# Performance work log

Hardware: AMD Instinct MI355X
Metric: run time of the kernel (lower is better)

The kernel has to match this reference:

```python
import jax, jax.numpy as jnp
import numpy as np

D = 1024          # input_dim
H = 16            # num_heads
S = 2             # scalar
MAX_LEN = 2048
HEAD_DIM = D // H // S      # 32
DV = D // H                 # 64, value head dim
SCALING = (D // H) ** -0.5


def setup_inputs() -> dict:
    key = jax.random.key(0)
    k1, k2, k3, k4, k5, k6 = jax.random.split(key, 6)
    L, B = 2046, 4
    input_tensor = jax.random.normal(k1, (L, B, D), dtype=jnp.float32)
    # k_v_proj: Linear(MAX_LEN, MAX_LEN // S); bias exists but is unused in forward
    w_kv = jax.random.normal(k2, (MAX_LEN // S, MAX_LEN), dtype=jnp.float32) / np.sqrt(MAX_LEN)
    # q_proj: Linear(D, D // S)
    w_q = jax.random.normal(k3, (D // S, D), dtype=jnp.float32) / np.sqrt(D)
    b_q = jax.random.normal(k4, (D // S,), dtype=jnp.float32) * 0.01
    # out_proj: Linear(D, D)
    w_out = jax.random.normal(k5, (D, D), dtype=jnp.float32) / np.sqrt(D)
    b_out = jax.random.normal(k6, (D,), dtype=jnp.float32) * 0.01
    return {"input_tensor": input_tensor, "w_kv": w_kv, "w_q": w_q,
            "b_q": b_q, "w_out": w_out, "b_out": b_out}


def reference(input_tensor, w_kv, w_q, b_q, w_out, b_out):
    L, B, _ = input_tensor.shape
    P = L // S + 1                       # projected (low-rank) sequence length
    X = jnp.transpose(input_tensor, (1, 0, 2))        # [B, L, D]
    q = X @ w_q.T + b_q                                # [B, L, D/S]
    Wp = w_kv.T[:L, :P]                                # [L, P] sequence projection
    v = jnp.einsum('bld,lp->bdp', X, Wp)               # [B, D, P]
    k = jnp.einsum('blc,lp->bcp', q, Wp)               # [B, D/S, P]
    q = q * SCALING
    # q: b l (h d) -> b h l d
    qh = q.reshape(B, L, H, HEAD_DIM).transpose(0, 2, 1, 3)
    # k: b (d h) p -> b h d p   (d outer, h inner in the channel split)
    kh = k.reshape(B, HEAD_DIM, H, P).transpose(0, 2, 1, 3)
    # v: b (d h) p -> b h p d
    vh = v.reshape(B, DV, H, P).transpose(0, 2, 3, 1)
    attn = jnp.einsum('bhld,bhdp->bhlp', qh, kh)       # [B, H, L, P]
    attn = jax.nn.softmax(attn.astype(jnp.float32), axis=-1).astype(attn.dtype)
    out = jnp.einsum('bhlp,bhpd->bhld', attn, vh)      # [B, H, L, DV]
    # (b h) l d -> b l (d h): d outer, h inner in concat
    out = out.transpose(0, 2, 3, 1).reshape(B, L, D)
    out = out @ w_out.T + b_out                        # [B, L, D]
    return jnp.transpose(out, (1, 0, 2))               # [L, B, D]
```

## Files before the change

kernel.cpp:

```cpp
#include <hip/hip_runtime.h>
#include <hip/hip_bf16.h>

typedef long long i64;
typedef unsigned int uint;
using u16 = unsigned short;
using f32x4  = __attribute__((ext_vector_type(4))) float;
using bf16x8 = __attribute__((ext_vector_type(8))) short;
using u32x4  = __attribute__((ext_vector_type(4))) uint;
using u16x4  = __attribute__((ext_vector_type(4))) u16;

#define QSCALE 0.18033688011112042f

#if __has_builtin(__builtin_amdgcn_exp2f)
#define EXP2(x) __builtin_amdgcn_exp2f(x)
#else
#define EXP2(x) __builtin_exp2f(x)
#endif

__device__ __forceinline__ u16 f2b(float x) {
    uint u = __float_as_uint(x);
    return (u16)((u + 0x7FFFu + ((u >> 16) & 1u)) >> 16);
}
__device__ __forceinline__ float b2f(u16 h) {
    return __uint_as_float((uint)h << 16);
}
__device__ __forceinline__ uint cvt_pk_bf16(float lo, float hi) {
    uint r;
    asm("v_cvt_pk_bf16_f32 %0, %1, %2" : "=v"(r) : "v"(lo), "v"(hi));
    return r;
}

__device__ __forceinline__ void conv_pad_dev(
    int bid, const float* __restrict__ src, u16* __restrict__ dst,
    int M_valid, int K_valid, int kshift, int s_row)
{
    i64 i = (i64)bid * 256 + threadIdx.x;
    int m = (int)(i >> (kshift - 2));
    int k = ((int)(i & ((1 << (kshift - 2)) - 1))) << 2;
    u16x4 hv;
    #pragma unroll
    for (int j = 0; j < 4; ++j) {
        int kk = k + j;
        float x = (m < M_valid && kk < K_valid) ? src[(i64)m * s_row + kk] : 0.f;
        hv[j] = f2b(x);
    }
    *(u16x4*)(dst + ((i64)m << kshift) + k) = hv;
}
__device__ __forceinline__ void conv_wout_dev(
    int bid, const float* __restrict__ w, u16* __restrict__ dst)
{
    int i = bid * 256 + threadIdx.x;
    int n = i >> 8, kp4 = (i & 255) << 2;
    u16x4 hv;
    #pragma unroll
    for (int j = 0; j < 4; ++j) {
        int kp = kp4 + j;
        hv[j] = f2b(w[((i64)n << 10) + ((kp & 63) << 4) + (kp >> 6)]);
    }
    *(u16x4*)(dst + ((i64)n << 10) + kp4) = hv;
}
__global__ __launch_bounds__(256) void conv_all(
    const float* __restrict__ X, const float* __restrict__ wq,
    const float* __restrict__ wkv, const float* __restrict__ wout,
    u16* __restrict__ Xb, u16* __restrict__ wq_b,
    u16* __restrict__ wkv_b, u16* __restrict__ wout_b)
{
    const int bid = blockIdx.x;
    if (bid < 8192)       conv_pad_dev(bid, X, Xb, 8184, 1024, 10, 1024);
    else if (bid < 8704)  conv_pad_dev(bid - 8192, wq, wq_b, 512, 1024, 10, 1024);
    else if (bid < 10752) conv_pad_dev(bid - 8704, wkv, wkv_b, 1024, 2046, 11, 2048);
    else                  conv_wout_dev(bid - 10752, wout, wout_b);
}

__global__ __launch_bounds__(256) void build_kvA(
    const u16* __restrict__ Xb, const u16* __restrict__ qu,
    u16* __restrict__ dst)
{
    const int b = blockIdx.z, r0 = blockIdx.y * 64, l0 = blockIdx.x * 64;
    const int tid = threadIdx.x;
    __shared__ float ts[64][65];
    #pragma unroll
    for (int t = 0; t < 16; ++t) {
        int idx = t * 256 + tid;
        int ch = idx & 63, lr = idx >> 6;
        int lg = l0 + lr;
        float v = 0.f;
        if (lg < 2046) {
            if (r0 < 1024) v = b2f(Xb[((i64)lg * 4 + b) * 1024 + (r0 + ch)]);
            else           v = b2f(qu[((i64)lg * 4 + b) * 512 + (r0 - 1024 + ch)]);
        }
        ts[lr][ch] = v;
    }
    __syncthreads();
    #pragma unroll
    for (int t = 0; t < 16; ++t) {
        int idx = t * 256 + tid;
        int ll = idx & 63, rl = idx >> 6;
        dst[((i64)b * 1536 + r0 + rl) * 2048 + l0 + ll] = f2b(ts[ll][rl]);
    }
}

template<int MODE>
__global__ __launch_bounds__(256) void gemm_bf16(
    const u16* __restrict__ A, i64 a_bs,
    const u16* __restrict__ Bm,
    float* __restrict__ C, const float* __restrict__ bias,
    u16* __restrict__ x0, u16* __restrict__ x1,
    int Krow, int KT, int M_valid)
{
    __shared__ __align__(16) u16 As[4096], Bs[8192];
    const int tid = threadIdx.x, lane = tid & 63, w = tid >> 6;
    const int fr = lane & 15, g = lane >> 4;

    const int fid = blockIdx.x;
    const int xcd = fid & 7, s = fid >> 3;
    int nb, mb, bz;
    if (MODE == 0)      { nb = xcd >> 1; mb = (xcd & 1) * 64 + s; bz = 0; }
    else if (MODE == 1) { nb = xcd; mb = s % 24; bz = s / 24; }
    else                { nb = xcd; mb = s & 31; bz = s >> 5; }

    const int srow = tid >> 3, sch = tid & 7;
    const int scol = (sch ^ (srow & 7)) << 3;
    const u16* Asrc = A + (i64)bz * a_bs + ((i64)mb * 64 + srow) * Krow + scol;
    const u16* Bsrc = Bm + ((i64)nb * 128 + srow) * Krow + scol;
    char* Adst = (char*)As + srow * 128 + sch * 16;
    char* Bdst = (char*)Bs + srow * 128 + sch * 16;

    f32x4 acc[2][4];
    #pragma unroll
    for (int i = 0; i < 2; ++i)
        #pragma unroll
        for (int j = 0; j < 4; ++j)
            acc[i][j] = (f32x4){0.f, 0.f, 0.f, 0.f};

    u32x4 st[6];
    st[0] = *(const u32x4*)(Asrc);
    st[1] = *(const u32x4*)(Asrc + (i64)32 * Krow);
    #pragma unroll
    for (int it = 0; it < 4; ++it)
        st[2 + it] = *(const u32x4*)(Bsrc + (i64)(it * 32) * Krow);

    const int wr = (w & 1) * 32, wc = (w >> 1) * 64;

    for (int kt = 0; kt < KT; ++kt) {
        __syncthreads();
        *(u32x4*)(Adst) = st[0];
        *(u32x4*)(Adst + 32 * 128) = st[1];
        #pragma unroll
        for (int it = 0; it < 4; ++it)
            *(u32x4*)(Bdst + it * 32 * 128) = st[2 + it];
        __syncthreads();
        if (kt + 1 < KT) {
            st[0] = *(const u32x4*)(Asrc + (kt + 1) * 64);
            st[1] = *(const u32x4*)(Asrc + (i64)32 * Krow + (kt + 1) * 64);
            #pragma unroll
            for (int it = 0; it < 4; ++it)
                st[2 + it] = *(const u32x4*)(Bsrc + (i64)(it * 32) * Krow
                                                  + (kt + 1) * 64);
        }
        #pragma unroll
        for (int half = 0; half < 2; ++half) {
            bf16x8 ah[2], bh[4];
            #pragma unroll
            for (int mi = 0; mi < 2; ++mi) {
                int rr = wr + mi * 16 + fr;
                ah[mi] = *(const bf16x8*)((const char*)As + rr * 128
                                          + (((half * 4 + g) ^ (rr & 7)) << 4));
            }
            #pragma unroll
            for (int ni = 0; ni < 4; ++ni) {
                int rr = wc + ni * 16 + fr;
                bh[ni] = *(const bf16x8*)((const char*)Bs + rr * 128
                                          + (((half * 4 + g) ^ (rr & 7)) << 4));
            }
            #pragma unroll
            for (int mi = 0; mi < 2; ++mi)
                #pragma unroll
                for (int ni = 0; ni < 4; ++ni)
                    acc[mi][ni] = __builtin_amdgcn_mfma_f32_16x16x32_bf16(
                        ah[mi], bh[ni], acc[mi][ni], 0, 0, 0);
        }
    }

    #pragma unroll
    for (int mi = 0; mi < 2; ++mi)
        #pragma unroll
        for (int ni = 0; ni < 4; ++ni) {
            int gm0 = mb * 64 + wr + mi * 16 + g * 4;
            int gn  = nb * 128 + wc + ni * 16 + fr;
            #pragma unroll
            for (int r = 0; r < 4; ++r) {
                int gm = gm0 + r;
                float val = acc[mi][ni][r];
                if (MODE == 0) {
                    x0[(i64)gm * 512 + gn] = f2b(val + bias[gn]);
                } else if (MODE == 1) {
                    if (gm < 1024) {
                        int e = gm >> 4, hh = gm & 15;
                        i64 so = ((i64)(bz * 16 + hh) * 64 + e) * 1024
                               + (gn & ~31) + (((gn >> 2) & 3) << 3)
                               + (gn & 3) + (((gn >> 4) & 1) << 2);
                        x1[so] = f2b(val);
                    } else {
                        int c2 = gm - 1024, d = c2 >> 4, hh = c2 & 15;
                        x0[((i64)(bz * 16 + hh) * 1024 + gn) * 32 + d] = f2b(val);
                    }
                } else {
                    if (gm < M_valid)
                        C[(i64)bz * 1024 + (i64)gm * 4096 + gn] = val + bias[gn];
                }
            }
        }
}

__global__ __launch_bounds__(256) void attn_mfma(
    const u16* __restrict__ qu, const u16* __restrict__ kT,
    const u16* __restrict__ vT, u16* __restrict__ attA)
{
    const int g0 = blockIdx.x;
    const int xcd = g0 & 7, sub = g0 >> 3;
    const int lblk = sub & 15;
    const int bh = xcd + ((sub >> 4) << 3);
    const int b = bh >> 4, h = bh & 15;
    const int tid = threadIdx.x, lane = tid & 63, w = tid >> 6;
    const int fr = lane & 15, g = lane >> 4;
    const int l0 = lblk * 128 + w * 32;

    __shared__ __align__(16) u16 kbuf[2][2048];
    __shared__ __align__(16) u16 vbuf[2][4096];

    bf16x8 aq[2];
    #pragma unroll
    for (int mf = 0; mf < 2; ++mf)
        aq[mf] = *(const bf16x8*)(qu + ((i64)((l0 + mf * 16 + fr) * 4 + b) * 512
                                        + h * 32 + g * 8));

    const f32x4 zf = {0.f, 0.f, 0.f, 0.f};

    const int sr = tid >> 2, sc = tid & 3;
    const u16* ksrc = kT + (i64)bh * 32768 + sr * 32
                    + ((sc ^ ((sr >> 1) & 3)) << 3);
    char* kdst = (char*)&kbuf[0][0] + tid * 16;
    const int vr = tid >> 3, vs = tid & 7;
    const u16* vsrc = vT + (i64)bh * 65536 + (i64)vr * 1024
                    + ((vs ^ (vr & 7)) << 3);
    char* vdst = (char*)&vbuf[0][0] + tid * 16;

    *(u32x4*)kdst = *(const u32x4*)ksrc;
    *(u32x4*)vdst = *(const u32x4*)vsrc;
    *(u32x4*)(vdst + 4096) = *(const u32x4*)(vsrc + 32 * 1024);
    __syncthreads();

    float l_part[2] = {0.f, 0.f};
    f32x4 o[2][4];
    #pragma unroll
    for (int mf = 0; mf < 2; ++mf)
        #pragma unroll
        for (int nf = 0; nf < 4; ++nf)
            o[mf][nf] = zf;

    const int kxor = (fr >> 1) & 3;
    const int vxor = fr & 7;

    #pragma unroll
    for (int t = 0; t < 16; ++t) {
        const int cur = t & 1;
        const int tn = (t < 15) ? t + 1 : 15;

        u32x4 knx  = *(const u32x4*)(ksrc + tn * 2048);
        u32x4 vnx0 = *(const u32x4*)(vsrc + tn * 64);
        u32x4 vnx1 = *(const u32x4*)(vsrc + 32 * 1024 + tn * 64);

        const char* kc_ = (const char*)&kbuf[cur][0];
        f32x4 s[2][4];
        __builtin_amdgcn_s_setprio(1);
        #pragma unroll
        for (int nf = 0; nf < 4; ++nf) {
            int row = nf * 16 + fr;
            bf16x8 ak = *(const bf16x8*)(kc_ + row * 64 + ((g ^ kxor) << 4));
            s[0][nf] = __builtin_amdgcn_mfma_f32_16x16x32_bf16(ak, aq[0], zf, 0, 0, 0);
            s[1][nf] = __builtin_amdgcn_mfma_f32_16x16x32_bf16(ak, aq[1], zf, 0, 0, 0);
        }
        __builtin_amdgcn_s_setprio(0);

        u32x4 ppk[2][2];
        #pragma unroll
        for (int mf = 0; mf < 2; ++mf)
            #pragma unroll
            for (int nf = 0; nf < 4; ++nf) {
                float p_[4];
                #pragma unroll
                for (int r = 0; r < 4; ++r) p_[r] = EXP2(QSCALE * s[mf][nf][r]);
                l_part[mf] += (p_[0] + p_[1]) + (p_[2] + p_[3]);
                ppk[mf][nf >> 1][(nf & 1) * 2 + 0] = cvt_pk_bf16(p_[0], p_[1]);
                ppk[mf][nf >> 1][(nf & 1) * 2 + 1] = cvt_pk_bf16(p_[2], p_[3]);
            }

        {
            const int nb_ = cur ^ 1;
            *(u32x4*)(kdst + nb_ * 4096) = knx;
            *(u32x4*)(vdst + nb_ * 8192) = vnx0;
            *(u32x4*)(vdst + nb_ * 8192 + 4096) = vnx1;
        }

        const char* vc_ = (const char*)&vbuf[cur][0];
        __builtin_amdgcn_s_setprio(1);
        #pragma unroll
        for (int ks = 0; ks < 2; ++ks) {
            bf16x8 ap0 = __builtin_bit_cast(bf16x8, ppk[0][ks]);
            bf16x8 ap1 = __builtin_bit_cast(bf16x8, ppk[1][ks]);
            const int slot = ((ks << 2) | g) ^ vxor;
            #pragma unroll
            for (int nf = 0; nf < 4; ++nf) {
                int row = nf * 16 + fr;
                bf16x8 bv = *(const bf16x8*)(vc_ + row * 128 + (slot << 4));
                o[0][nf] = __builtin_amdgcn_mfma_f32_16x16x32_bf16(ap0, bv, o[0][nf], 0, 0, 0);
                o[1][nf] = __builtin_amdgcn_mfma_f32_16x16x32_bf16(ap1, bv, o[1][nf], 0, 0, 0);
            }
        }
        __builtin_amdgcn_s_setprio(0);

        __syncthreads();
    }

    #pragma unroll
    for (int mf = 0; mf < 2; ++mf) {
        l_part[mf] += __shfl_xor(l_part[mf], 16);
        l_part[mf] += __shfl_xor(l_part[mf], 32);
    }
    #pragma unroll
    for (int mf = 0; mf < 2; ++mf)
        #pragma unroll
        for (int r = 0; r < 4; ++r) {
            int l = l0 + mf * 16 + g * 4 + r;
            float tot = __shfl(l_part[mf], g * 4 + r);
            if (l < 2046) {
                float inv = 1.f / tot;
                #pragma unroll
                for (int nf = 0; nf < 4; ++nf)
                    attA[((i64)b * 2048 + l) * 1024 + h * 64 + nf * 16 + fr]
                        = f2b(o[mf][nf][r] * inv);
            }
        }
}

extern "C" void kernel_launch(void* const* d_in, const int* in_sizes, int n_in,
                              void* d_out, int out_size, void* d_ws, size_t ws_size,
                              hipStream_t stream) {
    const float* input = (const float*)d_in[0];
    const float* w_kv  = (const float*)d_in[1];
    const float* w_q   = (const float*)d_in[2];
    const float* b_q   = (const float*)d_in[3];
    const float* w_out = (const float*)d_in[4];
    const float* b_out = (const float*)d_in[5];
    float* out = (float*)d_out;

    char* W = (char*)d_ws;
    u16* Xb      = (u16*)(W + 16777216);
    u16* qu      = (u16*)(W + 33554432);
    u16* wq_b    = (u16*)(W + 41943040);
    u16* wkv_b   = (u16*)(W + 42991616);
    u16* wout_b  = (u16*)(W + 47185920);
    u16* kvA     = (u16*)(W + 49283072);
    u16* kT      = (u16*)(W + 74448896);
    u16* vT      = (u16*)(W + 78643200);
    u16* attA    = (u16*)(W + 87031808);

    dim3 blk(256);

    conv_all<<<dim3(11776), blk, 0, stream>>>(
        input, w_q, w_kv, w_out, Xb, wq_b, wkv_b, wout_b);

    gemm_bf16<0><<<dim3(512), blk, 0, stream>>>(
        Xb, 0, wq_b, nullptr, b_q, qu, nullptr, 1024, 16, 8192);

    build_kvA<<<dim3(32, 24, 4), blk, 0, stream>>>(Xb, qu, kvA);

    gemm_bf16<1><<<dim3(768), blk, 0, stream>>>(
        kvA, (i64)1536 * 2048, wkv_b, nullptr, nullptr, kT, vT, 2048, 32, 1536);

    attn_mfma<<<dim3(1024), blk, 0, stream>>>(qu, kT, vT, attA);

    gemm_bf16<2><<<dim3(1024), blk, 0, stream>>>(
        attA, (i64)2048 * 1024, wout_b, out, b_out, nullptr, nullptr, 1024, 16, 2046);
}
```

Before: 160.9 us.

## Process two K/V tiles per barrier in attention loop with deeper prefetch

The attention kernel's K/V staging loop now handles two 64-column tiles per iteration. LDS buffers are doubled to hold two tiles per stage, prefetch loads fetch two tiles ahead, and the loop body is factored into a lambda. This halves the number of __syncthreads barriers and gives global loads more compute to hide behind. In exchange it uses twice the shared memory and more registers for in-flight prefetch data, which may reduce occupancy.

Measured after the change: 162.3 us. About the same (+0.9%).

```diff
diff --git a/kernel.cpp b/kernel.cpp
--- a/kernel.cpp
+++ b/kernel.cpp
@@ -226,8 +226,8 @@
     const int fr = lane & 15, g = lane >> 4;
     const int l0 = lblk * 128 + w * 32;
 
-    __shared__ __align__(16) u16 kbuf[2][2048];
-    __shared__ __align__(16) u16 vbuf[2][4096];
+    __shared__ __align__(16) u16 kbuf[2][2][2048];
+    __shared__ __align__(16) u16 vbuf[2][2][4096];
 
     bf16x8 aq[2];
     #pragma unroll
@@ -240,15 +240,18 @@
     const int sr = tid >> 2, sc = tid & 3;
     const u16* ksrc = kT + (i64)bh * 32768 + sr * 32
                     + ((sc ^ ((sr >> 1) & 3)) << 3);
-    char* kdst = (char*)&kbuf[0][0] + tid * 16;
+    char* kdst = (char*)&kbuf[0][0][0] + tid * 16;
     const int vr = tid >> 3, vs = tid & 7;
     const u16* vsrc = vT + (i64)bh * 65536 + (i64)vr * 1024
                     + ((vs ^ (vr & 7)) << 3);
-    char* vdst = (char*)&vbuf[0][0] + tid * 16;
-
-    *(u32x4*)kdst = *(const u32x4*)ksrc;
-    *(u32x4*)vdst = *(const u32x4*)vsrc;
-    *(u32x4*)(vdst + 4096) = *(const u32x4*)(vsrc + 32 * 1024);
+    char* vdst = (char*)&vbuf[0][0][0] + tid * 16;
+
+    *(u32x4*)(kdst)              = *(const u32x4*)(ksrc);
+    *(u32x4*)(kdst + 4096)       = *(const u32x4*)(ksrc + 2048);
+    *(u32x4*)(vdst)              = *(const u32x4*)(vsrc);
+    *(u32x4*)(vdst + 4096)       = *(const u32x4*)(vsrc + 32 * 1024);
+    *(u32x4*)(vdst + 8192)       = *(const u32x4*)(vsrc + 64);
+    *(u32x4*)(vdst + 8192 + 4096) = *(const u32x4*)(vsrc + 32 * 1024 + 64);
     __syncthreads();
 
     float l_part[2] = {0.f, 0.f};
@@ -262,16 +265,7 @@
     const int kxor = (fr >> 1) & 3;
     const int vxor = fr & 7;
 
-    #pragma unroll
-    for (int t = 0; t < 16; ++t) {
-        const int cur = t & 1;
-        const int tn = (t < 15) ? t + 1 : 15;
-
-        u32x4 knx  = *(const u32x4*)(ksrc + tn * 2048);
-        u32x4 vnx0 = *(const u32x4*)(vsrc + tn * 64);
-        u32x4 vnx1 = *(const u32x4*)(vsrc + 32 * 1024 + tn * 64);
-
-        const char* kc_ = (const char*)&kbuf[cur][0];
+    auto tilec = [&](const char* kc_, const char* vc_) {
         f32x4 s[2][4];
         __builtin_amdgcn_s_setprio(1);
         #pragma unroll
@@ -296,14 +290,6 @@
                 ppk[mf][nf >> 1][(nf & 1) * 2 + 1] = cvt_pk_bf16(p_[2], p_[3]);
             }
 
-        {
-            const int nb_ = cur ^ 1;
-            *(u32x4*)(kdst + nb_ * 4096) = knx;
-            *(u32x4*)(vdst + nb_ * 8192) = vnx0;
-            *(u32x4*)(vdst + nb_ * 8192 + 4096) = vnx1;
-        }
-
-        const char* vc_ = (const char*)&vbuf[cur][0];
         __builtin_amdgcn_s_setprio(1);
         #pragma unroll
         for (int ks = 0; ks < 2; ++ks) {
@@ -319,6 +305,38 @@
             }
         }
         __builtin_amdgcn_s_setprio(0);
+    };
+
+    #pragma unroll
+    for (int r = 0; r < 8; ++r) {
+        const int cur = r & 1;
+
+        u32x4 pk0, pk1, pv0a, pv0b, pv1a, pv1b;
+        if (r < 7) {
+            const int tp0 = 2 * r + 2, tp1 = 2 * r + 3;
+            pk0  = *(const u32x4*)(ksrc + tp0 * 2048);
+            pk1  = *(const u32x4*)(ksrc + tp1 * 2048);
+            pv0a = *(const u32x4*)(vsrc + tp0 * 64);
+            pv0b = *(const u32x4*)(vsrc + 32 * 1024 + tp0 * 64);
+            pv1a = *(const u32x4*)(vsrc + tp1 * 64);
+            pv1b = *(const u32x4*)(vsrc + 32 * 1024 + tp1 * 64);
+        }
+
+        tilec((const char*)&kbuf[0][0][0] + cur * 8192,
+              (const char*)&vbuf[0][0][0] + cur * 16384);
+
+        if (r < 7) {
+            const int nb_ = cur ^ 1;
+            *(u32x4*)(kdst + nb_ * 8192)               = pk0;
+            *(u32x4*)(kdst + nb_ * 8192 + 4096)        = pk1;
+            *(u32x4*)(vdst + nb_ * 16384)              = pv0a;
+            *(u32x4*)(vdst + nb_ * 16384 + 4096)       = pv0b;
+            *(u32x4*)(vdst + nb_ * 16384 + 8192)       = pv1a;
+            *(u32x4*)(vdst + nb_ * 16384 + 8192 + 4096) = pv1b;
+        }
+
+        tilec((const char*)&kbuf[0][0][0] + cur * 8192 + 4096,
+              (const char*)&vbuf[0][0][0] + cur * 16384 + 8192);
 
         __syncthreads();
     }
```
